# Kernel optimization log

Hardware: AMD Instinct MI355X
Metric: run time of the kernel (lower is better)

The kernel has to match this reference:

```python
import jax, jax.numpy as jnp
import numpy as np

NB = 32          # graph_batch_size
NEG_SLOPE = 0.2  # GATv2Conv leaky_relu slope


def _gat_spatial(X, V_Adap, Wl, bl, Wr, br, att, we, gat_bias, Wfc, bfc):
    # X: (B,T,N,F). GATv2 runs per time step on G diagonal blocks of size NB.
    B, T, N, F = X.shape
    G = N // NB
    Xb = X.reshape(B, T, G, NB, F)
    gl = jnp.einsum('btgnf,cf->btgnc', Xb, Wl) + bl  # lin_l (source msgs)
    gr = jnp.einsum('btgnf,cf->btgnc', Xb, Wr) + br  # lin_r (target)
    # diagonal blocks of the learned adjacency logits
    idx = jnp.arange(G)
    Vg = V_Adap[0].reshape(G, NB, G, NB)[idx, :, idx, :]   # (G, j_src, i_tgt)
    attr = jax.nn.sigmoid(Vg)                              # all > 0 => dense edges
    eye = jnp.eye(NB, dtype=bool)
    # PyG: remove self loops, then add self loops with fill_value='mean'
    off = jnp.where(eye, 0.0, attr)
    self_attr = off.sum(axis=1) / (NB - 1)                 # mean incoming per target
    attr_eff = jnp.where(eye, self_attr[:, None, :], attr) # (G, j, i)
    ef = attr_eff[..., None] * we                          # lin_edge, (G,j,i,C)
    ef = jnp.swapaxes(ef, 1, 2)                            # (G,i,j,C)
    # edges only cover flattened node ids 0..NB-1 => attention only for sample 0
    gl0, gr0 = gl[0], gr[0]                                # (T,G,NB,C)
    pre = gl0[:, :, None, :, :] + gr0[:, :, :, None, :] + ef[None]  # (T,G,i,j,C)
    S = jnp.einsum('tgijc,c->tgij', jax.nn.leaky_relu(pre, NEG_SLOPE), att)
    alpha = jax.nn.softmax(S, axis=-1)                     # softmax over sources j
    out0 = jnp.einsum('tgij,tgjc->tgic', alpha, gl0)
    # samples b>0: only the self loop -> alpha=1, message = gl
    out = jnp.concatenate([out0[None], gl[1:]], axis=0) + gat_bias
    y = jnp.einsum('btgnc,oc->btgno', out, Wfc) + bfc      # per-node fc
    return y.reshape(B, T, -1)                             # (B,T,N*spatial_out)


def _lstm_layer(x, Wih, Whh, bih, bhh):
    # torch LSTM gate order: i, f, g, o
    B, T, _ = x.shape
    H = Whh.shape[1]
    xg = jnp.einsum('bti,gi->btg', x, Wih) + bih           # (B,T,4H)
    xg = jnp.swapaxes(xg, 0, 1)                            # (T,B,4H)

    def step(carry, xt):
        h, c = carry
        g = xt + h @ Whh.T + bhh
        i, f, gg, o = jnp.split(g, 4, axis=-1)
        i = jax.nn.sigmoid(i)
        f = jax.nn.sigmoid(f)
        gg = jnp.tanh(gg)
        o = jax.nn.sigmoid(o)
        c = f * c + i * gg
        h = o * jnp.tanh(c)
        return (h, c), h

    h0 = jnp.zeros((B, H), x.dtype)
    _, hs = jax.lax.scan(step, (h0, h0), xg)
    return jnp.swapaxes(hs, 0, 1)                          # (B,T,H)


def setup_inputs() -> dict:
    key = jax.random.key(0)
    ks = jax.random.split(key, 24)
    B, T, N, F = 8, 64, 256, 64
    C, O, NC, H, HL = 128, 32, 16, 1024, 2
    s = 0.05
    inp = {
        'X': jax.random.normal(ks[0], (B, T, N, F), jnp.float32),
        'V_Adap': 0.2 + 0.05 * jax.random.normal(ks[1], (1, N, N), jnp.float32),
        'Wl': s * jax.random.normal(ks[2], (C, F), jnp.float32),
        'bl': s * jax.random.normal(ks[3], (C,), jnp.float32),
        'Wr': s * jax.random.normal(ks[4], (C, F), jnp.float32),
        'br': s * jax.random.normal(ks[5], (C,), jnp.float32),
        'att': s * jax.random.normal(ks[6], (C,), jnp.float32),
        'we': s * jax.random.normal(ks[7], (C,), jnp.float32),
        'gat_bias': s * jax.random.normal(ks[8], (C,), jnp.float32),
        'Wfc': s * jax.random.normal(ks[9], (O, C), jnp.float32),
        'bfc': s * jax.random.normal(ks[10], (O,), jnp.float32),
        'Wih0': s * jax.random.normal(ks[11], (4 * H, N * O), jnp.float32),
        'Whh0': s * jax.random.normal(ks[12], (4 * H, H), jnp.float32),
        'bih0': s * jax.random.normal(ks[13], (4 * H,), jnp.float32),
        'bhh0': s * jax.random.normal(ks[14], (4 * H,), jnp.float32),
        'Wih1': s * jax.random.normal(ks[15], (4 * H, H), jnp.float32),
        'Whh1': s * jax.random.normal(ks[16], (4 * H, H), jnp.float32),
        'bih1': s * jax.random.normal(ks[17], (4 * H,), jnp.float32),
        'bhh1': s * jax.random.normal(ks[18], (4 * H,), jnp.float32),
        'Wout': s * jax.random.normal(ks[19], (NC, H), jnp.float32),
        'bout': s * jax.random.normal(ks[20], (NC,), jnp.float32),
    }
    return inp


def reference(X, V_Adap, Wl, bl, Wr, br, att, we, gat_bias, Wfc, bfc,
              Wih0, Whh0, bih0, bhh0, Wih1, Whh1, bih1, bhh1, Wout, bout):
    s = _gat_spatial(X, V_Adap, Wl, bl, Wr, br, att, we, gat_bias, Wfc, bfc)
    h1 = _lstm_layer(s, Wih0, Whh0, bih0, bhh0)
    h2 = _lstm_layer(h1, Wih1, Whh1, bih1, bhh1)
    return h2[:, -1, :] @ Wout.T + bout                    # (B, num_classes)
```

## Files before the change

### kernel.cpp

```cpp
#include <hip/hip_runtime.h>
#include <cmath>

#define B_ 8
#define T_ 64
#define N_ 256
#define F_ 64
#define C_ 128
#define O_ 32
#define H_ 1024
#define NC_ 16

typedef __attribute__((ext_vector_type(8))) short bf16x8;
typedef __attribute__((ext_vector_type(4))) float f32x4;

__device__ __forceinline__ float sigf(float x){ return 1.f/(1.f+expf(-x)); }

__device__ __forceinline__ unsigned short f2bf(float f){
  unsigned int u = __float_as_uint(f);
  u += 0x7fff + ((u >> 16) & 1);
  return (unsigned short)(u >> 16);
}
__device__ __forceinline__ float bf2f(unsigned short s){
  return __uint_as_float(((unsigned int)s) << 16);
}

__device__ __forceinline__ void gload16(const void* g, void* l){
  __builtin_amdgcn_global_load_lds((const __attribute__((address_space(1))) void*)g,
                                   (__attribute__((address_space(3))) void*)l, 16, 0, 0);
}

__device__ __forceinline__ bf16x8 cvt8(const float* p){
  float4 a = *(const float4*)p, b = *(const float4*)(p + 4);
  bf16x8 r;
  r[0] = (short)f2bf(a.x); r[1] = (short)f2bf(a.y);
  r[2] = (short)f2bf(a.z); r[3] = (short)f2bf(a.w);
  r[4] = (short)f2bf(b.x); r[5] = (short)f2bf(b.y);
  r[6] = (short)f2bf(b.z); r[7] = (short)f2bf(b.w);
  return r;
}

#define TAGW(l, b) ((((l)*128) + (b)) << 5)
#define NTAGW 8192

__global__ __launch_bounds__(256) void attr_kernel(const float* __restrict__ V, float* __restrict__ attr){
  __shared__ float sv[32][33];
  __shared__ float selfv[32];
  int g = blockIdx.x, tid = threadIdx.x;
  for (int idx = tid; idx < 1024; idx += 256){
    int j = idx >> 5, i = idx & 31;
    sv[j][i] = sigf(V[(size_t)(g*32 + j)*256 + g*32 + i]);
  }
  __syncthreads();
  if (tid < 32){
    float s = 0.f;
    for (int j = 0; j < 32; ++j) if (j != tid) s += sv[j][tid];
    selfv[tid] = s * (1.f/31.f);
  }
  __syncthreads();
  for (int idx = tid; idx < 1024; idx += 256){
    int j = idx >> 5, i = idx & 31;
    attr[g*1024 + idx] = (j == i) ? selfv[i] : sv[j][i];
  }
}

__global__ __launch_bounds__(256) void prep_kernel(
    const float* __restrict__ Wl, const float* __restrict__ Wr,
    const float* __restrict__ bl, const float* __restrict__ gb,
    const float* __restrict__ Wfc, const float* __restrict__ bfc,
    unsigned short* __restrict__ wcomb,
    float* __restrict__ bias_comb,
    unsigned short* __restrict__ wlr){
  __shared__ float wls[8192], wfcs[4096];
  int tid = threadIdx.x;
  for (int i = tid; i < 8192; i += 256) wls[i] = Wl[i];
  for (int i = tid; i < 4096; i += 256) wfcs[i] = Wfc[i];
  __syncthreads();
  for (int idx = tid; idx < 2048; idx += 256){
    int o = idx >> 6, f = idx & 63;
    float acc = 0.f;
    for (int c = 0; c < 128; ++c) acc = fmaf(wfcs[o*128 + c], wls[c*64 + f], acc);
    wcomb[idx] = f2bf(acc);
  }
  if (tid < 32){
    float acc = bfc[tid];
    for (int c = 0; c < 128; ++c) acc = fmaf(wfcs[tid*128 + c], bl[c] + gb[c], acc);
    bias_comb[tid] = acc;
  }
  for (int idx = tid; idx < 16384; idx += 256){
    int r = idx >> 6, f = idx & 63;
    wlr[idx] = f2bf(r < 128 ? wls[r*64 + f] : Wr[(r-128)*64 + f]);
  }
}

__global__ __launch_bounds__(256) void gemm_proj0(
    const float* __restrict__ X, const unsigned short* __restrict__ wlr,
    const float* __restrict__ bl, const float* __restrict__ br,
    float* __restrict__ gl0, float* __restrict__ gr0){
  int tid = threadIdx.x;
  int lane = tid & 63, w = tid >> 6;
  int lr = lane & 15, ko = lane >> 4;
  int row = blockIdx.x*64 + w*16 + lr;

  bf16x8 af[2];
  #pragma unroll
  for (int ks = 0; ks < 2; ++ks)
    af[ks] = cvt8(&X[(size_t)row*64 + ks*32 + ko*8]);

  f32x4 zero = {0.f,0.f,0.f,0.f};
  #pragma unroll 4
  for (int nt = 0; nt < 16; ++nt){
    f32x4 acc = zero;
    #pragma unroll
    for (int ks = 0; ks < 2; ++ks){
      bf16x8 bv = *(const bf16x8*)&wlr[(size_t)(nt*16 + lr)*64 + ks*32 + ko*8];
      acc = __builtin_amdgcn_mfma_f32_16x16x32_bf16(af[ks], bv, acc, 0, 0, 0);
    }
    int col = nt*16 + lr;
    #pragma unroll
    for (int v = 0; v < 4; ++v){
      int orow = blockIdx.x*64 + w*16 + ko*4 + v;
      if (col < 128) gl0[(size_t)orow*128 + col]        = acc[v] + bl[col];
      else           gr0[(size_t)orow*128 + (col-128)]  = acc[v] + br[col-128];
    }
  }
}

__global__ __launch_bounds__(256) void gemm_rest(
    const float* __restrict__ X, const unsigned short* __restrict__ wcomb,
    const float* __restrict__ bias_comb, unsigned short* __restrict__ xl){
  int tid = threadIdx.x;
  int lane = tid & 63, w = tid >> 6;
  int lr = lane & 15, ko = lane >> 4;
  int r0 = 16384 + blockIdx.x*256 + w*64;

  bf16x8 bv[2][2];
  #pragma unroll
  for (int nt = 0; nt < 2; ++nt)
    #pragma unroll
    for (int ks = 0; ks < 2; ++ks)
      bv[nt][ks] = *(const bf16x8*)&wcomb[(size_t)(nt*16 + lr)*64 + ks*32 + ko*8];

  f32x4 zero = {0.f,0.f,0.f,0.f};
  #pragma unroll
  for (int mt = 0; mt < 4; ++mt){
    int row = r0 + mt*16 + lr;
    bf16x8 af[2];
    #pragma unroll
    for (int ks = 0; ks < 2; ++ks)
      af[ks] = cvt8(&X[(size_t)row*64 + ks*32 + ko*8]);
    f32x4 acc0 = zero, acc1 = zero;
    #pragma unroll
    for (int ks = 0; ks < 2; ++ks){
      acc0 = __builtin_amdgcn_mfma_f32_16x16x32_bf16(af[ks], bv[0][ks], acc0, 0, 0, 0);
      acc1 = __builtin_amdgcn_mfma_f32_16x16x32_bf16(af[ks], bv[1][ks], acc1, 0, 0, 0);
    }
    #pragma unroll
    for (int v = 0; v < 4; ++v){
      int orow = r0 + mt*16 + ko*4 + v;
      xl[(size_t)orow*32 + lr]      = f2bf(acc0[v] + bias_comb[lr]);
      xl[(size_t)orow*32 + 16 + lr] = f2bf(acc1[v] + bias_comb[16 + lr]);
    }
  }
}

__global__ __launch_bounds__(256) void attn_kernel(
    const float* __restrict__ gl0, const float* __restrict__ gr0,
    const float* __restrict__ attr, const float* __restrict__ we, const float* __restrict__ att,
    const float* __restrict__ gbias, const float* __restrict__ Wfc, const float* __restrict__ bfc,
    unsigned short* __restrict__ xl){
  __shared__ float gls[32*129], grs[32*129], os_[32*129], Wfcs[32*129];
  __shared__ float ae[32*33], Ss[32*33];
  __shared__ float wes[128], atts[128];
  int tid = threadIdx.x, blk = blockIdx.x;
  int g = blk & 7, t = blk >> 3;

  const float* glp = gl0 + ((size_t)t*N_ + g*32)*C_;
  const float* grp = gr0 + ((size_t)t*N_ + g*32)*C_;
  for (int idx = tid; idx < 4096; idx += 256){
    int n = idx >> 7, c = idx & 127;
    gls[n*129 + c]  = glp[idx];
    grs[n*129 + c]  = grp[idx];
    Wfcs[n*129 + c] = Wfc[idx];
  }
  for (int idx = tid; idx < 1024; idx += 256) ae[(idx>>5)*33 + (idx&31)] = attr[g*1024 + idx];
  if (tid < 128){ wes[tid] = we[tid]; atts[tid] = att[tid]; }
  __syncthreads();

  int i = tid >> 3, jb = (tid & 7) * 4;
  float a0 = ae[(jb+0)*33 + i], a1 = ae[(jb+1)*33 + i], a2 = ae[(jb+2)*33 + i], a3 = ae[(jb+3)*33 + i];
  float s0 = 0.f, s1 = 0.f, s2 = 0.f, s3 = 0.f;
  for (int cc = 0; cc < 128; ++cc){
    float grv = grs[i*129 + cc];
    float wv = wes[cc], av = atts[cc];
    float p0 = gls[(jb+0)*129 + cc] + grv + a0*wv;
    float p1 = gls[(jb+1)*129 + cc] + grv + a1*wv;
    float p2 = gls[(jb+2)*129 + cc] + grv + a2*wv;
    float p3 = gls[(jb+3)*129 + cc] + grv + a3*wv;
    p0 = p0 > 0.f ? p0 : 0.2f*p0;
    p1 = p1 > 0.f ? p1 : 0.2f*p1;
    p2 = p2 > 0.f ? p2 : 0.2f*p2;
    p3 = p3 > 0.f ? p3 : 0.2f*p3;
    s0 = fmaf(p0, av, s0); s1 = fmaf(p1, av, s1);
    s2 = fmaf(p2, av, s2); s3 = fmaf(p3, av, s3);
  }
  Ss[i*33 + jb + 0] = s0; Ss[i*33 + jb + 1] = s1;
  Ss[i*33 + jb + 2] = s2; Ss[i*33 + jb + 3] = s3;
  __syncthreads();

  if (tid < 32){
    float mx = -1e30f;
    for (int j = 0; j < 32; ++j) mx = fmaxf(mx, Ss[tid*33 + j]);
    float sum = 0.f;
    for (int j = 0; j < 32; ++j) sum += expf(Ss[tid*33 + j] - mx);
    float inv = 1.f / sum;
    for (int j = 0; j < 32; ++j) Ss[tid*33 + j] = expf(Ss[tid*33 + j] - mx) * inv;
  }
  __syncthreads();

  int c2 = tid & 127, ibase = (tid >> 7) * 16;
  float gbv = gbias[c2];
  for (int p = 0; p < 16; ++p){
    int ii = ibase + p;
    float acc = 0.f;
    #pragma unroll
    for (int j = 0; j < 32; ++j) acc = fmaf(Ss[ii*33 + j], gls[j*129 + c2], acc);
    os_[ii*129 + c2] = acc + gbv;
  }
  __syncthreads();

  int o = tid & 31, n2b = tid >> 5;
  float bfv = bfc[o];
  for (int p = 0; p < 4; ++p){
    int n2 = n2b + 8*p;
    float acc = bfv;
    for (int cc = 0; cc < 128; ++cc)
      acc = fmaf(os_[n2*129 + cc], Wfcs[o*129 + cc], acc);
    xl[((size_t)t*N_ + g*32 + n2)*O_ + o] = f2bf(acc);
  }
}

__global__ __launch_bounds__(256) void f2b_kernel(const float* __restrict__ in,
                                                  unsigned short* __restrict__ out, int n4){
  int idx = blockIdx.x*256 + threadIdx.x;
  if (idx >= n4) return;
  float4 v = ((const float4*)in)[idx];
  ushort4 o;
  o.x = f2bf(v.x); o.y = f2bf(v.y); o.z = f2bf(v.z); o.w = f2bf(v.w);
  ((ushort4*)out)[idx] = o;
}

__global__ __launch_bounds__(256) void w2cat_kernel(const float* __restrict__ Whh1,
                                                    const float* __restrict__ Wih1,
                                                    unsigned short* __restrict__ w2){
  int row = blockIdx.x, tid = threadIdx.x;
  const float* a = Whh1 + (size_t)row*1024 + tid*4;
  const float* b = Wih1 + (size_t)row*1024 + tid*4;
  float4 va = *(const float4*)a, vb = *(const float4*)b;
  ushort4 oa, ob;
  oa.x = f2bf(va.x); oa.y = f2bf(va.y); oa.z = f2bf(va.z); oa.w = f2bf(va.w);
  ob.x = f2bf(vb.x); ob.y = f2bf(vb.y); ob.z = f2bf(vb.z); ob.w = f2bf(vb.w);
  *(ushort4*)&w2[(size_t)row*2048 + tid*4]        = oa;
  *(ushort4*)&w2[(size_t)row*2048 + 1024 + tid*4] = ob;
}

__global__ __launch_bounds__(256) void gemm_bf2s(
    const unsigned short* __restrict__ A, const unsigned short* __restrict__ W,
    float* __restrict__ Yp, int N, int K){
  __shared__ __align__(16) short As[2][64*64];
  __shared__ __align__(16) short Bs[2][128*64];
  int tid = threadIdx.x;
  int id = blockIdx.x;
  int ks = id >> 8, rest = id & 255;
  int xcd = rest & 7, local = rest >> 3;
  int nt = xcd*4 + (local & 3), mt = local >> 2;
  int m0 = mt*64, n0 = nt*128;
  int kbase = ks * (K >> 1);
  float* Y = Yp + (size_t)ks*512*N;
  int lane = tid & 63;
  int w = tid >> 6, wm = w >> 1, wn = w & 1;
  int lr = lane & 15, ko = lane >> 4;
  int wbase = tid & ~63;

  auto STAGE = [&](int buf, int kc){
    #pragma unroll
    for (int it = 0; it < 2; ++it){
      int chunk = it*256 + tid;
      int r = chunk >> 3, c8 = chunk & 7;
      int cs = (c8 ^ (r & 7)) << 3;
      gload16(&A[(size_t)(m0 + r)*K + kc + cs], &As[buf][(size_t)(it*256 + wbase)*8]);
    }
    #pragma unroll
    for (int it = 0; it < 4; ++it){
      int chunk = it*256 + tid;
      int r = chunk >> 3, c8 = chunk & 7;
      int cs = (c8 ^ (r & 7)) << 3;
      gload16(&W[(size_t)(n0 + r)*K + kc + cs], &Bs[buf][(size_t)(it*256 + wbase)*8]);
    }
  };

  f32x4 zero = {0.f,0.f,0.f,0.f};
  f32x4 acc[2][4] = {{zero,zero,zero,zero},{zero,zero,zero,zero}};

  STAGE(0, kbase);
  __syncthreads();
  int nk = K >> 7;
  for (int kt = 0; kt < nk; ++kt){
    int cur = kt & 1;
    if (kt + 1 < nk) STAGE(cur ^ 1, kbase + ((kt + 1) << 6));
    #pragma unroll
    for (int kk = 0; kk < 2; ++kk){
      int s = kk*4 + ko;
      bf16x8 af[2], bfv[4];
      #pragma unroll
      for (int m = 0; m < 2; ++m){
        int row = wm*32 + m*16 + lr;
        af[m] = *(const bf16x8*)&As[cur][row*64 + ((s ^ (row & 7)) << 3)];
      }
      #pragma unroll
      for (int n = 0; n < 4; ++n){
        int row = wn*64 + n*16 + lr;
        bfv[n] = *(const bf16x8*)&Bs[cur][row*64 + ((s ^ (row & 7)) << 3)];
      }
      #pragma unroll
      for (int m = 0; m < 2; ++m)
        #pragma unroll
        for (int n = 0; n < 4; ++n)
          acc[m][n] = __builtin_amdgcn_mfma_f32_16x16x32_bf16(af[m], bfv[n], acc[m][n], 0, 0, 0);
    }
    __syncthreads();
  }

  #pragma unroll
  for (int m = 0; m < 2; ++m)
    #pragma unroll
    for (int n = 0; n < 4; ++n)
      #pragma unroll
      for (int v = 0; v < 4; ++v){
        int row = m0 + wm*32 + m*16 + ko*4 + v;
        int col = n0 + wn*64 + n*16 + lr;
        Y[(size_t)row*N + col] = acc[m][n][v];
      }
}

__global__ __launch_bounds__(256) void ksum_kernel(
    const float* __restrict__ p0, const float* __restrict__ p1,
    const float* __restrict__ b1, const float* __restrict__ b2,
    float* __restrict__ Y, unsigned* __restrict__ syncw){
  int idx = blockIdx.x*256 + threadIdx.x;
  if (idx < NTAGW) syncw[idx] = 0u;
  int i4 = idx;
  float4 a = ((const float4*)p0)[i4];
  float4 b = ((const float4*)p1)[i4];
  int col = (i4 << 2) & 4095;
  float4 u = *(const float4*)&b1[col];
  float4 v = *(const float4*)&b2[col];
  float4 o;
  o.x = a.x + b.x + u.x + v.x;
  o.y = a.y + b.y + u.y + v.y;
  o.z = a.z + b.z + u.z + v.z;
  o.w = a.w + b.w + u.w + v.w;
  ((float4*)Y)[i4] = o;
}

__global__ __launch_bounds__(512) void lstm_persist(
    const unsigned short* __restrict__ whh0,
    const unsigned short* __restrict__ w2cat,
    const float* __restrict__ xg0,
    const float* __restrict__ bih1, const float* __restrict__ bhh1,
    unsigned short* __restrict__ h1seq,
    unsigned short* __restrict__ h2seq,
    unsigned* __restrict__ syncw){
  __shared__ float red[2][4][8][64];
  const int tid = threadIdx.x;
  const int lane = tid & 63, w = tid >> 6;
  const int g = w >> 2, ws = w & 3;
  const bool layer2 = (blockIdx.x >= 128);
  const int lb = layer2 ? (int)blockIdx.x - 128 : (int)blockIdx.x;
  const int lr = lane & 15, ko = lane >> 4;
  const int q = lr >> 2, dl = lr & 3;
  const int row = q*H_ + lb*8 + g*4 + dl;

  bf16x8 wreg[16];
  if (!layer2){
    const unsigned short* wrow = whh0 + (size_t)row*1024 + ws*256;
    #pragma unroll
    for (int kk = 0; kk < 8; ++kk) wreg[kk] = *(const bf16x8*)&wrow[kk*32 + ko*8];
  } else {
    const unsigned short* wrow = w2cat + (size_t)row*2048 + ws*512;
    #pragma unroll
    for (int kk = 0; kk < 16; ++kk) wreg[kk] = *(const bf16x8*)&wrow[kk*32 + ko*8];
  }

  const int g2 = tid >> 5, bt = (tid >> 2) & 7, dl2 = tid & 3;
  const int dimt = lb*8 + g2*4 + dl2;
  float creg = 0.f;
  float b2r[4] = {0.f,0.f,0.f,0.f};
  if (layer2 && tid < 64){
    #pragma unroll
    for (int qq = 0; qq < 4; ++qq) b2r[qq] = bih1[qq*H_ + dimt] + bhh1[qq*H_ + dimt];
  }
  const bf16x8 zero8 = {0,0,0,0,0,0,0,0};
  const int ttend = layer2 ? 64 : 63;

  for (int tt = 0; tt <= ttend; ++tt){
    const int tau = layer2 ? tt - 1 : tt;
    const bool active = layer2 ? (tt >= 1) : true;
    const int par = tt & 1;

    {
      int base = -1, cnt = 0, need = 0;
      if (!layer2){
        if (tt > 0){ base = ws*32; cnt = 32; need = tt; }
      } else if (tt >= 1){
        if (ws < 2){ if (tau >= 1){ base = 128 + ws*64; cnt = 64; need = tau; } }
        else        {               base = (ws-2)*64;   cnt = 64; need = tau+1; }
      }
      if (base >= 0){
        unsigned* tp = syncw + ((size_t)(base + (lane & (cnt-1))) << 5);
        for (;;){
          unsigned v = __hip_atomic_load(tp, __ATOMIC_RELAXED, __HIP_MEMORY_SCOPE_AGENT);
          if (__all(v >= (unsigned)need)) break;
          __builtin_amdgcn_s_sleep(1);
        }
      }
    }

    f32x4 accv = {0.f,0.f,0.f,0.f};
    if (active){
      const unsigned short* arow = nullptr;
      if (!layer2){
        if (tt > 0) arow = h1seq + ((size_t)(lr & 7)*T_ + (tt-1))*H_ + ws*256;
      } else {
        if (ws < 2){ if (tau > 0) arow = h2seq + ((size_t)(lr & 7)*T_ + (tau-1))*H_ + ws*512; }
        else         arow = h1seq + ((size_t)(lr & 7)*T_ + tau)*H_ + (ws-2)*512;
      }
      if (arow){
        f32x4 acc2 = {0.f,0.f,0.f,0.f};
        if (!layer2){
          #pragma unroll
          for (int kk = 0; kk < 8; ++kk){
            bf16x8 av = (lr < 8) ? *(const bf16x8*)&arow[kk*32 + ko*8] : zero8;
            if (kk & 1) acc2 = __builtin_amdgcn_mfma_f32_16x16x32_bf16(av, wreg[kk], acc2, 0, 0, 0);
            else        accv = __builtin_amdgcn_mfma_f32_16x16x32_bf16(av, wreg[kk], accv, 0, 0, 0);
          }
        } else {
          #pragma unroll
          for (int kk = 0; kk < 16; ++kk){
            bf16x8 av = (lr < 8) ? *(const bf16x8*)&arow[kk*32 + ko*8] : zero8;
            if (kk & 1) acc2 = __builtin_amdgcn_mfma_f32_16x16x32_bf16(av, wreg[kk], acc2, 0, 0, 0);
            else        accv = __builtin_amdgcn_mfma_f32_16x16x32_bf16(av, wreg[kk], accv, 0, 0, 0);
          }
        }
        accv = accv + acc2;
      }
    }
    #pragma unroll
    for (int v = 0; v < 4; ++v) red[par][v][w][lane] = accv[v];
    __syncthreads();

    if (active && w == 0){
      float pre[4];
      #pragma unroll
      for (int qq = 0; qq < 4; ++qq){
        int lsrc = (bt >> 2)*16 + qq*4 + dl2, v = bt & 3;
        pre[qq] = red[par][v][g2*4+0][lsrc] + red[par][v][g2*4+1][lsrc]
                + red[par][v][g2*4+2][lsrc] + red[par][v][g2*4+3][lsrc];
      }
      float pi, pf, pg, po;
      if (!layer2){
        size_t xb = ((size_t)bt*T_ + tt)*4096;
        pi = pre[0] + xg0[xb + 0*H_ + dimt];
        pf = pre[1] + xg0[xb + 1*H_ + dimt];
        pg = pre[2] + xg0[xb + 2*H_ + dimt];
        po = pre[3] + xg0[xb + 3*H_ + dimt];
      } else {
        pi = pre[0] + b2r[0]; pf = pre[1] + b2r[1];
        pg = pre[2] + b2r[2]; po = pre[3] + b2r[3];
      }
      float i_ = sigf(pi), f_ = sigf(pf), g_ = tanhf(pg), o_ = sigf(po);
      float cn = fmaf(f_, creg, i_*g_);
      creg = cn;
      float hn = o_ * tanhf(cn);
      unsigned short* hp = (layer2 ? h2seq : h1seq) + ((size_t)bt*T_ + tau)*H_ + dimt;
      __hip_atomic_store(hp, f2bf(hn), __ATOMIC_RELAXED, __HIP_MEMORY_SCOPE_AGENT);
      asm volatile("s_waitcnt vmcnt(0)" ::: "memory");
      if (lane == 0){
        const int fl = layer2 ? 1 : 0;
        __hip_atomic_store(syncw + TAGW(fl, lb), (unsigned)((layer2 ? tau : tt) + 1),
                           __ATOMIC_RELAXED, __HIP_MEMORY_SCOPE_AGENT);
      }
    }
  }
}

__global__ __launch_bounds__(128) void final_kernel(
    const unsigned short* __restrict__ h2_seq, const float* __restrict__ Wout,
    const float* __restrict__ bout, float* __restrict__ out){
  int tid = threadIdx.x;
  int b = tid >> 4, nc = tid & 15;
  const unsigned short* hp = h2_seq + ((size_t)b*T_ + (T_ - 1))*H_;
  const float* wp = Wout + nc*H_;
  float acc = bout[nc];
  for (int k = 0; k < 1024; ++k) acc = fmaf(bf2f(hp[k]), wp[k], acc);
  out[tid] = acc;
}

extern "C" void kernel_launch(void* const* d_in, const int* in_sizes, int n_in,
                              void* d_out, int out_size, void* d_ws, size_t ws_size,
                              hipStream_t stream){
  const float* X    = (const float*)d_in[0];
  const float* V    = (const float*)d_in[1];
  const float* Wl   = (const float*)d_in[2];
  const float* bl   = (const float*)d_in[3];
  const float* Wr   = (const float*)d_in[4];
  const float* br   = (const float*)d_in[5];
  const float* att  = (const float*)d_in[6];
  const float* we   = (const float*)d_in[7];
  const float* gb   = (const float*)d_in[8];
  const float* Wfc  = (const float*)d_in[9];
  const float* bfc  = (const float*)d_in[10];
  const float* Wih0 = (const float*)d_in[11];
  const float* Whh0 = (const float*)d_in[12];
  const float* bih0 = (const float*)d_in[13];
  const float* bhh0 = (const float*)d_in[14];
  const float* Wih1 = (const float*)d_in[15];
  const float* Whh1 = (const float*)d_in[16];
  const float* bih1 = (const float*)d_in[17];
  const float* bhh1 = (const float*)d_in[18];
  const float* Wout = (const float*)d_in[19];
  const float* bout = (const float*)d_in[20];

  float* ws   = (float*)d_ws;
  float* attr = ws;
  float* gl0  = attr + 8192;
  float* gr0  = gl0 + 2097152;
  float* xg0  = gr0 + 2097152;
  float* bias_comb = xg0 + 2097152;
  unsigned short* xl_bf  = (unsigned short*)(bias_comb + 64);
  unsigned short* w0_bf  = xl_bf + 4194304;
  unsigned short* wh0_bf = w0_bf + 33554432;
  unsigned short* w2_bf  = wh0_bf + 4194304;
  unsigned short* h1_bf  = w2_bf + 8388608;
  unsigned short* h2_bf  = h1_bf + 524288;
  unsigned short* wlr_bf = h2_bf + 524288;
  unsigned short* wcomb  = wlr_bf + 16384;
  unsigned* syncw = (unsigned*)xl_bf;
  (void)in_sizes; (void)n_in; (void)out_size; (void)ws_size;

  attr_kernel<<<8, 256, 0, stream>>>(V, attr);
  prep_kernel<<<1, 256, 0, stream>>>(Wl, Wr, bl, gb, Wfc, bfc, wcomb, bias_comb, wlr_bf);
  gemm_proj0<<<256, 256, 0, stream>>>(X, wlr_bf, bl, br, gl0, gr0);
  attn_kernel<<<512, 256, 0, stream>>>(gl0, gr0, attr, we, att, gb, Wfc, bfc, xl_bf);
  gemm_rest<<<448, 256, 0, stream>>>(X, wcomb, bias_comb, xl_bf);

  f2b_kernel<<<32768, 256, 0, stream>>>(Wih0, w0_bf, 8388608);
  f2b_kernel<<<4096, 256, 0, stream>>>(Whh0, wh0_bf, 1048576);
  w2cat_kernel<<<4096, 256, 0, stream>>>(Whh1, Wih1, w2_bf);

  gemm_bf2s<<<512, 256, 0, stream>>>(xl_bf, w0_bf, gl0, 4096, 8192);
  ksum_kernel<<<2048, 256, 0, stream>>>(gl0, gr0, bih0, bhh0, xg0, syncw);

  {
    void* args[] = {(void*)&wh0_bf, (void*)&w2_bf, (void*)&xg0,
                    (void*)&bih1, (void*)&bhh1, (void*)&h1_bf, (void*)&h2_bf,
                    (void*)&syncw};
    hipLaunchCooperativeKernel((const void*)lstm_persist, dim3(256), dim3(512),
                               args, 0, stream);
  }

  final_kernel<<<1, 128, 0, stream>>>(h2_bf, Wout, bout, (float*)d_out);
}
```

Measured before the change: 660.8 us.

## Repartition persistent LSTM across fewer blocks with full-K waves and shuffle-based gates

The persistent LSTM kernel shrinks from 256 to 96 blocks: layer 1 uses 32 blocks where each wave holds the full K=1024 of its weight rows, and layer 2 uses 64 blocks with a two-way K split. Gate math now uses lane shuffles on MFMA outputs instead of an LDS reduction (layer 1 needs no LDS reduction at all). Cross-block sync polls far fewer flags, with one wave polling and then releasing the rest through LDS flags. The aim is lower per-step sync and reduction latency in the serial recurrence, at the cost of more weight registers per wave (32 bf16x8 vectors) and fewer CUs doing the matmul.

After: 943.1 us. 1.43x slower.

```diff
diff --git a/kernel.cpp b/kernel.cpp
--- a/kernel.cpp
+++ b/kernel.cpp
@@ -39,8 +39,8 @@
   return r;
 }
 
-#define TAGW(l, b) ((((l)*128) + (b)) << 5)
-#define NTAGW 8192
+#define TAGW(i) ((i) << 5)
+#define NTAGW 3072
 
 __global__ __launch_bounds__(256) void attr_kernel(const float* __restrict__ V, float* __restrict__ attr){
   __shared__ float sv[32][33];
@@ -362,7 +362,7 @@
   ((float4*)Y)[i4] = o;
 }
 
-__global__ __launch_bounds__(512) void lstm_persist(
+__global__ __launch_bounds__(512, 2) void lstm_persist(
     const unsigned short* __restrict__ whh0,
     const unsigned short* __restrict__ w2cat,
     const float* __restrict__ xg0,
@@ -370,125 +370,153 @@
     unsigned short* __restrict__ h1seq,
     unsigned short* __restrict__ h2seq,
     unsigned* __restrict__ syncw){
-  __shared__ float red[2][4][8][64];
+  __shared__ float red[2][8][64][4];
+  __shared__ volatile unsigned goS;
+  __shared__ volatile unsigned doneS[8];
   const int tid = threadIdx.x;
   const int lane = tid & 63, w = tid >> 6;
-  const int g = w >> 2, ws = w & 3;
-  const bool layer2 = (blockIdx.x >= 128);
-  const int lb = layer2 ? (int)blockIdx.x - 128 : (int)blockIdx.x;
-  const int lr = lane & 15, ko = lane >> 4;
-  const int q = lr >> 2, dl = lr & 3;
-  const int row = q*H_ + lb*8 + g*4 + dl;
-
-  bf16x8 wreg[16];
+  const bool layer2 = (blockIdx.x >= 32);
+  const int lb = layer2 ? (int)blockIdx.x - 32 : (int)blockIdx.x;
+  const int r = lane & 15, ko = lane >> 4;
+  const int q = r >> 2, dl = r & 3;
+  const bf16x8 zero8 = {0,0,0,0,0,0,0,0};
+
+  if (tid == 0){ goS = 0u; for (int i = 0; i < 8; ++i) doneS[i] = 0u; }
+  __syncthreads();
+
+  bf16x8 wreg[32];
+  int dimw;
   if (!layer2){
-    const unsigned short* wrow = whh0 + (size_t)row*1024 + ws*256;
-    #pragma unroll
-    for (int kk = 0; kk < 8; ++kk) wreg[kk] = *(const bf16x8*)&wrow[kk*32 + ko*8];
+    dimw = lb*32 + w*4 + dl;
+    const unsigned short* wrow = whh0 + (size_t)(q*H_ + dimw)*1024;
+    #pragma unroll
+    for (int kk = 0; kk < 32; ++kk) wreg[kk] = *(const bf16x8*)&wrow[kk*32 + ko*8];
   } else {
-    const unsigned short* wrow = w2cat + (size_t)row*2048 + ws*512;
-    #pragma unroll
-    for (int kk = 0; kk < 16; ++kk) wreg[kk] = *(const bf16x8*)&wrow[kk*32 + ko*8];
-  }
-
-  const int g2 = tid >> 5, bt = (tid >> 2) & 7, dl2 = tid & 3;
-  const int dimt = lb*8 + g2*4 + dl2;
-  float creg = 0.f;
-  float b2r[4] = {0.f,0.f,0.f,0.f};
-  if (layer2 && tid < 64){
-    #pragma unroll
-    for (int qq = 0; qq < 4; ++qq) b2r[qq] = bih1[qq*H_ + dimt] + bhh1[qq*H_ + dimt];
-  }
-  const bf16x8 zero8 = {0,0,0,0,0,0,0,0};
-  const int ttend = layer2 ? 64 : 63;
-
-  for (int tt = 0; tt <= ttend; ++tt){
+    const int rgp = w & 3, kc = w >> 2;
+    dimw = lb*16 + rgp*4 + dl;
+    const unsigned short* wrow = w2cat + (size_t)(q*H_ + dimw)*2048 + kc*1024;
+    #pragma unroll
+    for (int kk = 0; kk < 32; ++kk) wreg[kk] = *(const bf16x8*)&wrow[kk*32 + ko*8];
+  }
+  float b2v = 0.f;
+  if (layer2) b2v = bih1[q*H_ + dimw] + bhh1[q*H_ + dimw];
+
+  const int rg = lane >> 4;
+  f32x4 cregv = {0.f,0.f,0.f,0.f};
+  const int kc2 = w >> 2;
+
+  const int tt0 = layer2 ? 1 : 0;
+  const int tt1 = layer2 ? 64 : 63;
+
+  for (int tt = tt0; tt <= tt1; ++tt){
     const int tau = layer2 ? tt - 1 : tt;
-    const bool active = layer2 ? (tt >= 1) : true;
     const int par = tt & 1;
 
+    float xgv[4] = {0.f,0.f,0.f,0.f};
+    if (!layer2 && rg < 2){
+      #pragma unroll
+      for (int v = 0; v < 4; ++v)
+        xgv[v] = xg0[((size_t)(rg*4 + v)*T_ + tt)*4096 + q*H_ + dimw];
+    }
+
+    if (w == 0){
+      bool need = layer2 || (tt > 0);
+      if (need){
+        unsigned* pA = 0; unsigned nA = 0;
+        unsigned* pB = 0; unsigned nB = 0;
+        if (!layer2){
+          if (lane < 32){ pA = syncw + TAGW(lane); nA = (unsigned)tt; }
+        } else {
+          if (lane < 32){ pA = syncw + TAGW(lane); nA = (unsigned)tt; }
+          if (tt >= 2) { pB = syncw + TAGW(32 + lane); nB = (unsigned)(tt-1);}
+        }
+        for (;;){
+          bool ok = true;
+          if (pA) ok = (__hip_atomic_load(pA, __ATOMIC_RELAXED, __HIP_MEMORY_SCOPE_AGENT) >= nA);
+          if (ok && pB) ok = (__hip_atomic_load(pB, __ATOMIC_RELAXED, __HIP_MEMORY_SCOPE_AGENT) >= nB);
+          if (__all(ok)) break;
+          __builtin_amdgcn_s_sleep(2);
+        }
+      }
+      if (lane == 0) goS = (unsigned)(tt + 1);
+    } else {
+      while (goS < (unsigned)(tt + 1)) __builtin_amdgcn_s_sleep(1);
+    }
+
+    f32x4 accv = {0.f,0.f,0.f,0.f};
     {
-      int base = -1, cnt = 0, need = 0;
-      if (!layer2){
-        if (tt > 0){ base = ws*32; cnt = 32; need = tt; }
-      } else if (tt >= 1){
-        if (ws < 2){ if (tau >= 1){ base = 128 + ws*64; cnt = 64; need = tau; } }
-        else        {               base = (ws-2)*64;   cnt = 64; need = tau+1; }
-      }
-      if (base >= 0){
-        unsigned* tp = syncw + ((size_t)(base + (lane & (cnt-1))) << 5);
-        for (;;){
-          unsigned v = __hip_atomic_load(tp, __ATOMIC_RELAXED, __HIP_MEMORY_SCOPE_AGENT);
-          if (__all(v >= (unsigned)need)) break;
-          __builtin_amdgcn_s_sleep(1);
-        }
-      }
-    }
-
-    f32x4 accv = {0.f,0.f,0.f,0.f};
-    if (active){
       const unsigned short* arow = nullptr;
       if (!layer2){
-        if (tt > 0) arow = h1seq + ((size_t)(lr & 7)*T_ + (tt-1))*H_ + ws*256;
+        if (tt > 0) arow = h1seq + ((size_t)(r & 7)*T_ + (tt-1))*H_;
       } else {
-        if (ws < 2){ if (tau > 0) arow = h2seq + ((size_t)(lr & 7)*T_ + (tau-1))*H_ + ws*512; }
-        else         arow = h1seq + ((size_t)(lr & 7)*T_ + tau)*H_ + (ws-2)*512;
+        if (kc2 == 0){ if (tau > 0) arow = h2seq + ((size_t)(r & 7)*T_ + (tau-1))*H_; }
+        else          arow = h1seq + ((size_t)(r & 7)*T_ + tau)*H_;
       }
       if (arow){
         f32x4 acc2 = {0.f,0.f,0.f,0.f};
-        if (!layer2){
-          #pragma unroll
-          for (int kk = 0; kk < 8; ++kk){
-            bf16x8 av = (lr < 8) ? *(const bf16x8*)&arow[kk*32 + ko*8] : zero8;
-            if (kk & 1) acc2 = __builtin_amdgcn_mfma_f32_16x16x32_bf16(av, wreg[kk], acc2, 0, 0, 0);
-            else        accv = __builtin_amdgcn_mfma_f32_16x16x32_bf16(av, wreg[kk], accv, 0, 0, 0);
-          }
-        } else {
-          #pragma unroll
-          for (int kk = 0; kk < 16; ++kk){
-            bf16x8 av = (lr < 8) ? *(const bf16x8*)&arow[kk*32 + ko*8] : zero8;
-            if (kk & 1) acc2 = __builtin_amdgcn_mfma_f32_16x16x32_bf16(av, wreg[kk], acc2, 0, 0, 0);
-            else        accv = __builtin_amdgcn_mfma_f32_16x16x32_bf16(av, wreg[kk], accv, 0, 0, 0);
-          }
+        #pragma unroll
+        for (int kk = 0; kk < 32; ++kk){
+          bf16x8 av = (r < 8) ? *(const bf16x8*)&arow[kk*32 + ko*8] : zero8;
+          if (kk & 1) acc2 = __builtin_amdgcn_mfma_f32_16x16x32_bf16(av, wreg[kk], acc2, 0, 0, 0);
+          else        accv = __builtin_amdgcn_mfma_f32_16x16x32_bf16(av, wreg[kk], accv, 0, 0, 0);
         }
         accv = accv + acc2;
       }
     }
-    #pragma unroll
-    for (int v = 0; v < 4; ++v) red[par][v][w][lane] = accv[v];
-    __syncthreads();
-
-    if (active && w == 0){
-      float pre[4];
-      #pragma unroll
-      for (int qq = 0; qq < 4; ++qq){
-        int lsrc = (bt >> 2)*16 + qq*4 + dl2, v = bt & 3;
-        pre[qq] = red[par][v][g2*4+0][lsrc] + red[par][v][g2*4+1][lsrc]
-                + red[par][v][g2*4+2][lsrc] + red[par][v][g2*4+3][lsrc];
-      }
-      float pi, pf, pg, po;
-      if (!layer2){
-        size_t xb = ((size_t)bt*T_ + tt)*4096;
-        pi = pre[0] + xg0[xb + 0*H_ + dimt];
-        pf = pre[1] + xg0[xb + 1*H_ + dimt];
-        pg = pre[2] + xg0[xb + 2*H_ + dimt];
-        po = pre[3] + xg0[xb + 3*H_ + dimt];
-      } else {
-        pi = pre[0] + b2r[0]; pf = pre[1] + b2r[1];
-        pg = pre[2] + b2r[2]; po = pre[3] + b2r[3];
-      }
-      float i_ = sigf(pi), f_ = sigf(pf), g_ = tanhf(pg), o_ = sigf(po);
-      float cn = fmaf(f_, creg, i_*g_);
-      creg = cn;
-      float hn = o_ * tanhf(cn);
-      unsigned short* hp = (layer2 ? h2seq : h1seq) + ((size_t)bt*T_ + tau)*H_ + dimt;
-      __hip_atomic_store(hp, f2bf(hn), __ATOMIC_RELAXED, __HIP_MEMORY_SCOPE_AGENT);
+
+    bool do_gates;
+    f32x4 pre;
+    if (!layer2){
+      #pragma unroll
+      for (int v = 0; v < 4; ++v) pre[v] = accv[v] + xgv[v];
+      do_gates = true;
+    } else {
+      #pragma unroll
+      for (int v = 0; v < 4; ++v) red[par][w][lane][v] = accv[v];
+      __syncthreads();
+      if (w < 4){
+        #pragma unroll
+        for (int v = 0; v < 4; ++v)
+          pre[v] = red[par][w][lane][v] + red[par][w+4][lane][v] + b2v;
+        do_gates = true;
+      } else do_gates = false;
+    }
+
+    if (do_gates){
+      const int base = (lane & 48) | dl;
+      float pi[4], pf[4], pg[4], po[4];
+      #pragma unroll
+      for (int v = 0; v < 4; ++v){
+        pi[v] = __shfl(pre[v], base);
+        pf[v] = __shfl(pre[v], base | 4);
+        pg[v] = __shfl(pre[v], base | 8);
+        po[v] = __shfl(pre[v], base | 12);
+      }
+      if (r < 4 && rg < 2){
+        unsigned short* hdst = (layer2 ? h2seq : h1seq);
+        #pragma unroll
+        for (int v = 0; v < 4; ++v){
+          float i_ = sigf(pi[v]), f_ = sigf(pf[v]), g_ = tanhf(pg[v]), o_ = sigf(po[v]);
+          float cn = fmaf(f_, cregv[v], i_*g_);
+          cregv[v] = cn;
+          float hn = o_ * tanhf(cn);
+          __hip_atomic_store(&hdst[((size_t)(rg*4 + v)*T_ + tau)*H_ + dimw], f2bf(hn),
+                             __ATOMIC_RELAXED, __HIP_MEMORY_SCOPE_AGENT);
+        }
+      }
       asm volatile("s_waitcnt vmcnt(0)" ::: "memory");
-      if (lane == 0){
-        const int fl = layer2 ? 1 : 0;
-        __hip_atomic_store(syncw + TAGW(fl, lb), (unsigned)((layer2 ? tau : tt) + 1),
-                           __ATOMIC_RELAXED, __HIP_MEMORY_SCOPE_AGENT);
-      }
+      if (lane == 0) doneS[w] = (unsigned)(tt + 1);
+    }
+
+    if (w == 0){
+      const int nwv = layer2 ? 4 : 8;
+      bool ok;
+      do {
+        ok = (lane < nwv) ? (doneS[lane] >= (unsigned)(tt + 1)) : true;
+      } while (!__all(ok));
+      if (lane == 0)
+        __hip_atomic_store(syncw + TAGW(layer2 ? (32 + lb) : lb),
+                           (unsigned)(tau + 1), __ATOMIC_RELAXED, __HIP_MEMORY_SCOPE_AGENT);
     }
   }
 }
@@ -564,7 +592,7 @@
     void* args[] = {(void*)&wh0_bf, (void*)&w2_bf, (void*)&xg0,
                     (void*)&bih1, (void*)&bhh1, (void*)&h1_bf, (void*)&h2_bf,
                     (void*)&syncw};
-    hipLaunchCooperativeKernel((const void*)lstm_persist, dim3(256), dim3(512),
+    hipLaunchCooperativeKernel((const void*)lstm_persist, dim3(96), dim3(512),
                                args, 0, stream);
   }
 
```
